# Optimization experiments

Hardware: AMD Instinct MI355X
Metric: run time of the kernel (lower is better)

The kernel has to match this reference:

```python
import jax, jax.numpy as jnp
import numpy as np
import math

NUM_HEADS = 8
DIM = 512
DH = DIM // NUM_HEADS  # 64


def _rotary(x):
    # x: (b, l, h, s, d) ; interleaved-pair rotary (lucidrains RotaryEmbedding default)
    d = x.shape[-1]
    s = x.shape[-2]
    inv_freq = 1.0 / (10000.0 ** (jnp.arange(0, d, 2, dtype=jnp.float32) / d))  # (d/2,)
    t = jnp.arange(s, dtype=jnp.float32)
    freqs = t[:, None] * inv_freq[None, :]                # (s, d/2)
    freqs = jnp.repeat(freqs, 2, axis=-1)                 # (s, d) interleaved duplication
    cos = jnp.cos(freqs).astype(x.dtype)
    sin = jnp.sin(freqs).astype(x.dtype)
    x1 = x[..., 0::2]
    x2 = x[..., 1::2]
    rot = jnp.stack([-x2, x1], axis=-1).reshape(x.shape)  # rotate_half on interleaved pairs
    return x * cos + rot * sin


def setup_inputs() -> dict:
    key = jax.random.key(0)
    ks = jax.random.split(key, 9)
    b, l, s = 2, 2, 2048
    std = 1.0 / math.sqrt(DIM)
    inp = {
        "x": jax.random.normal(ks[0], (b, l, s, DIM), dtype=jnp.float32),
        "Wq": jax.random.normal(ks[1], (DIM, DIM), dtype=jnp.float32) * std,
        "bq": jnp.zeros((DIM,), dtype=jnp.float32),
        "Wk": jax.random.normal(ks[2], (DIM, DIM), dtype=jnp.float32) * std,
        "bk": jnp.zeros((DIM,), dtype=jnp.float32),
        "Wv": jax.random.normal(ks[3], (DIM, DIM), dtype=jnp.float32) * std,
        "bv": jnp.zeros((DIM,), dtype=jnp.float32),
        "Wo": jax.random.normal(ks[4], (DIM, DIM), dtype=jnp.float32) * std,
        "bo": jnp.zeros((DIM,), dtype=jnp.float32),
    }
    return inp


def reference(x, Wq, bq, Wk, bk, Wv, bv, Wo, bo):
    b, l, s, _ = x.shape
    h, dh = NUM_HEADS, DH

    def proj(W, bias):
        y = jnp.einsum('blsd,ed->blse', x, W) + bias      # nn.Linear: x @ W.T + b
        return y.reshape(b, l, s, h, dh).transpose(0, 1, 3, 2, 4)  # b l h s d

    q_proj = proj(Wq, bq)
    k_proj = proj(Wk, bk)
    v_proj = proj(Wv, bv)

    # Faithful to the source's swapped tuple unpack: k_mat <- V projection, v_mat <- K projection
    q_mat = _rotary(q_proj)
    k_mat = _rotary(v_proj)
    v_mat = k_proj

    scale = 1.0 / math.sqrt(dh * h)  # sqrt(dim), as in source
    scores = jnp.einsum('blhqd,blhkd->blhqk', q_mat, k_mat) * scale

    causal = jnp.tril(jnp.ones((s, s), dtype=bool))
    scores = jnp.where(causal[None, None, None], scores, -jnp.inf)

    weights = jax.nn.softmax(scores, axis=-1)
    inter = jnp.einsum('blhqk,blhkd->blhqd', weights, v_mat)
    inter = inter.transpose(0, 1, 3, 2, 4).reshape(b, l, s, h * dh)  # b l s (h d)
    out = jnp.einsum('blse,de->blsd', inter, Wo) + bo
    return out
```

## Files before the change

kernel.cpp:

```cpp
#include <hip/hip_runtime.h>
#include <math.h>

#define BB 2
#define LL 2
#define SS 2048
#define DD 512
#define HH 8
#define DHH 64

typedef __attribute__((ext_vector_type(8))) short bf16x8;
typedef __attribute__((ext_vector_type(4))) float f32x4;

#define MFMA16(a, b, c) __builtin_amdgcn_mfma_f32_16x16x32_bf16((a), (b), (c), 0, 0, 0)

__device__ __forceinline__ unsigned short f2bf(float f) {
    union { float f; unsigned u; } x; x.f = f;
    unsigned u = x.u;
    return (unsigned short)((u + 0x7fffu + ((u >> 16) & 1u)) >> 16);
}

__device__ __forceinline__ void gload16(const unsigned short* g, unsigned short* l) {
    __builtin_amdgcn_global_load_lds(
        (const __attribute__((address_space(1))) unsigned int*)g,
        (__attribute__((address_space(3))) unsigned int*)l, 16, 0, 0);
}

__global__ void rope_table_kernel(float* __restrict__ cos_t, float* __restrict__ sin_t) {
    int idx = blockIdx.x * 256 + threadIdx.x;
    if (idx >= SS * 32) return;
    int s = idx >> 5;
    int f = idx & 31;
    double inv = pow(10000.0, -(double)(2 * f) / (double)DHH);
    double ang = (double)s * inv;
    cos_t[idx] = (float)cos(ang);
    sin_t[idx] = (float)sin(ang);
}

__global__ __launch_bounds__(256) void convert_kernel(
    const float* __restrict__ x,  const float* __restrict__ wq,
    const float* __restrict__ wk, const float* __restrict__ wv,
    const float* __restrict__ wo, unsigned short* __restrict__ dst)
{
    int i = blockIdx.x * 256 + threadIdx.x;
    const float* src;
    int local;
    if (i < 1048576)      { src = x;  local = i; }
    else if (i < 1114112) { src = wq; local = i - 1048576; }
    else if (i < 1179648) { src = wk; local = i - 1114112; }
    else if (i < 1245184) { src = wv; local = i - 1179648; }
    else                  { src = wo; local = i - 1245184; }
    float4 v = ((const float4*)src)[local];
    ushort4 o;
    o.x = f2bf(v.x); o.y = f2bf(v.y); o.z = f2bf(v.z); o.w = f2bf(v.w);
    *(ushort4*)&dst[(size_t)i * 4] = o;
}

__global__ __launch_bounds__(256) void qkv_mfma_kernel(
    const unsigned short* __restrict__ xb,
    const unsigned short* __restrict__ wqb,
    const unsigned short* __restrict__ wkb,
    const unsigned short* __restrict__ wvb,
    const float* __restrict__ bq, const float* __restrict__ bk,
    const float* __restrict__ bv,
    const float* __restrict__ cos_t, const float* __restrict__ sin_t,
    unsigned short* __restrict__ qm, unsigned short* __restrict__ km,
    unsigned short* __restrict__ vt)
{
    __shared__ __align__(16) unsigned short As[4096];
    __shared__ __align__(16) unsigned short Bs[4096];

    const int tid  = threadIdx.x;
    const int w    = tid >> 6;
    const int lane = tid & 63;
    const int c    = lane & 15;
    const int quad = lane >> 4;
    const int mw   = (w & 1) * 64;
    const int nw   = (w >> 1) * 64;

    const int bx    = blockIdx.x;
    const int mat   = bx >> 2;
    const int nloc0 = (bx & 3) * 128;
    const int row0  = blockIdx.y * 128;

    const unsigned short* wsel = (mat == 0) ? wqb : (mat == 1) ? wkb : wvb;
    const float* bsel          = (mat == 0) ? bq  : (mat == 1) ? bk  : bv;

    const unsigned short* aSrc = (mat == 1) ? (wsel + (size_t)nloc0 * DD)
                                            : (xb   + (size_t)row0  * DD);
    const unsigned short* bSrc = (mat == 1) ? (xb   + (size_t)row0  * DD)
                                            : (wsel + (size_t)nloc0 * DD);

    f32x4 acc[4][4];
    #pragma unroll
    for (int i = 0; i < 4; ++i)
        #pragma unroll
        for (int j = 0; j < 4; ++j)
            #pragma unroll
            for (int r = 0; r < 4; ++r) acc[i][j][r] = 0.f;

    for (int k0 = 0; k0 < DD; k0 += 32) {
        __syncthreads();
        #pragma unroll
        for (int it = 0; it < 2; ++it) {
            int L   = it * 2048 + w * 512 + lane * 8;
            int row = L >> 5;
            int k   = L & 31;
            gload16(aSrc + (size_t)row * DD + k0 + k, &As[L]);
            gload16(bSrc + (size_t)row * DD + k0 + k, &Bs[L]);
        }
        __syncthreads();
        bf16x8 af[4], bfr[4];
        #pragma unroll
        for (int mt = 0; mt < 4; ++mt)
            af[mt] = *(const bf16x8*)&As[(mw + mt * 16 + c) * 32 + quad * 8];
        #pragma unroll
        for (int nt = 0; nt < 4; ++nt)
            bfr[nt] = *(const bf16x8*)&Bs[(nw + nt * 16 + c) * 32 + quad * 8];
        #pragma unroll
        for (int mt = 0; mt < 4; ++mt)
            #pragma unroll
            for (int nt = 0; nt < 4; ++nt)
                acc[mt][nt] = MFMA16(af[mt], bfr[nt], acc[mt][nt]);
    }

    if (mat == 1) {
        #pragma unroll
        for (int mt = 0; mt < 4; ++mt) {
            #pragma unroll
            for (int nt = 0; nt < 4; ++nt) {
                int xr = row0 + nw + nt * 16 + c;
                int bl = xr >> 11, s = xr & 2047;
                #pragma unroll
                for (int r = 0; r < 4; ++r) {
                    int col = nloc0 + mw + mt * 16 + quad * 4 + r;
                    int h = col >> 6, dh = col & 63;
                    float v = acc[mt][nt][r] + bsel[col];
                    vt[((size_t)(bl * HH + h) * DHH + dh) * SS + s] = f2bf(v);
                }
            }
        }
    } else {
        unsigned short* dst = (mat == 0) ? qm : km;
        const float qscale = (mat == 0) ? 0.04419417382415922f : 1.0f;
        #pragma unroll
        for (int mt = 0; mt < 4; ++mt) {
            #pragma unroll
            for (int r = 0; r < 4; ++r) {
                int xr = row0 + mw + mt * 16 + quad * 4 + r;
                int bl = xr >> 11, s = xr & 2047;
                #pragma unroll
                for (int nt = 0; nt < 4; ++nt) {
                    int col = nloc0 + nw + nt * 16 + c;
                    int h = col >> 6, dh = col & 63;
                    float v = acc[mt][nt][r] + bsel[col];
                    float pv = __shfl_xor(v, 1);
                    int f = dh >> 1;
                    float cs = cos_t[s * 32 + f], sn = sin_t[s * 32 + f];
                    float o = (dh & 1) ? fmaf(v, cs, pv * sn)
                                       : fmaf(v, cs, -(pv * sn));
                    dst[((size_t)(bl * HH + h) * SS + s) * DHH + dh] = f2bf(o * qscale);
                }
            }
        }
    }
}

#define S_KV 72
#define S_P  72

__global__ __launch_bounds__(256) void attn_mfma_kernel(
    const unsigned short* __restrict__ qm,
    const unsigned short* __restrict__ km,
    const unsigned short* __restrict__ vt,
    unsigned short* __restrict__ inter)
{
    __shared__ unsigned short Ks[64 * S_KV];
    __shared__ unsigned short Vt[64 * S_KV];
    __shared__ unsigned short Ps[128 * S_P];

    const int tid  = threadIdx.x;
    const int w    = tid >> 6;
    const int lane = tid & 63;
    const int c    = lane & 15;
    const int quad = lane >> 4;

    const int qt = (gridDim.x - 1) - blockIdx.x;
    const int h  = blockIdx.y;
    const int bl = blockIdx.z;
    const int q0 = qt * 128;
    const int qw = q0 + w * 32;

    const size_t seq_base = (size_t)(bl * HH + h) * SS * DHH;
    const size_t vt_base  = (size_t)(bl * HH + h) * DHH * SS;

    bf16x8 qf[2][2];
    #pragma unroll
    for (int mt = 0; mt < 2; ++mt)
        #pragma unroll
        for (int kk = 0; kk < 2; ++kk)
            qf[mt][kk] = *(const bf16x8*)(qm + seq_base +
                (size_t)(qw + mt * 16 + c) * DHH + kk * 32 + quad * 8);

    f32x4 oacc[4][2];
    f32x4 lacc[2];
    #pragma unroll
    for (int i = 0; i < 4; ++i)
        #pragma unroll
        for (int j = 0; j < 2; ++j)
            #pragma unroll
            for (int r = 0; r < 4; ++r) oacc[i][j][r] = 0.f;
    #pragma unroll
    for (int j = 0; j < 2; ++j)
        #pragma unroll
        for (int r = 0; r < 4; ++r) lacc[j][r] = 0.f;

    bf16x8 ones;
    #pragma unroll
    for (int i = 0; i < 8; ++i) ones[i] = (short)0x3F80;

    const int ntiles = 2 * qt + 2;
    for (int kt = 0; kt < ntiles; ++kt) {
        __syncthreads();
        {
            const unsigned short* kg = km + seq_base + (size_t)(kt * 64) * DHH;
            const unsigned short* vg = vt + vt_base + kt * 64;
            #pragma unroll
            for (int it = 0; it < 2; ++it) {
                int idx = tid + it * 256;
                int row = idx >> 3, ch = idx & 7;
                *(bf16x8*)&Ks[row * S_KV + ch * 8] = *(const bf16x8*)(kg + idx * 8);
                *(bf16x8*)&Vt[row * S_KV + ch * 8] =
                    *(const bf16x8*)(vg + (size_t)row * SS + ch * 8);
            }
        }
        __syncthreads();

        if (64 * kt <= qw + 31) {
            f32x4 sacc[2][4];
            #pragma unroll
            for (int mt = 0; mt < 2; ++mt)
                #pragma unroll
                for (int nt = 0; nt < 4; ++nt)
                    #pragma unroll
                    for (int r = 0; r < 4; ++r) sacc[mt][nt][r] = 0.f;
            #pragma unroll
            for (int kk = 0; kk < 2; ++kk) {
                bf16x8 bk_[4];
                #pragma unroll
                for (int nt = 0; nt < 4; ++nt)
                    bk_[nt] = *(const bf16x8*)&Ks[(nt * 16 + c) * S_KV + kk * 32 + quad * 8];
                #pragma unroll
                for (int mt = 0; mt < 2; ++mt)
                    #pragma unroll
                    for (int nt = 0; nt < 4; ++nt)
                        sacc[mt][nt] = MFMA16(qf[mt][kk], bk_[nt], sacc[mt][nt]);
            }

            const bool need_mask = (64 * kt + 63 > qw);
            #pragma unroll
            for (int mt = 0; mt < 2; ++mt) {
                #pragma unroll
                for (int r = 0; r < 4; ++r) {
                    int prow = w * 32 + mt * 16 + quad * 4 + r;
                    int qrow = qw + mt * 16 + quad * 4 + r;
                    unsigned short* pp = &Ps[prow * S_P + c];
                    #pragma unroll
                    for (int nt = 0; nt < 4; ++nt) {
                        float p = __expf(sacc[mt][nt][r]);
                        if (need_mask && (64 * kt + nt * 16 + c > qrow)) p = 0.f;
                        pp[nt * 16] = f2bf(p);
                    }
                }
            }

            #pragma unroll
            for (int kk = 0; kk < 2; ++kk) {
                bf16x8 bp0 = *(const bf16x8*)&Ps[(w * 32 + c) * S_P + kk * 32 + quad * 8];
                bf16x8 bp1 = *(const bf16x8*)&Ps[(w * 32 + 16 + c) * S_P + kk * 32 + quad * 8];
                lacc[0] = MFMA16(ones, bp0, lacc[0]);
                lacc[1] = MFMA16(ones, bp1, lacc[1]);
                #pragma unroll
                for (int mt4 = 0; mt4 < 4; ++mt4) {
                    bf16x8 av = *(const bf16x8*)&Vt[(mt4 * 16 + c) * S_KV + kk * 32 + quad * 8];
                    oacc[mt4][0] = MFMA16(av, bp0, oacc[mt4][0]);
                    oacc[mt4][1] = MFMA16(av, bp1, oacc[mt4][1]);
                }
            }
        }
    }

    float invl0 = 1.f / lacc[0][0];
    float invl1 = 1.f / lacc[1][0];
    #pragma unroll
    for (int mt4 = 0; mt4 < 4; ++mt4) {
        int dh0 = mt4 * 16 + quad * 4;
        #pragma unroll
        for (int nt2 = 0; nt2 < 2; ++nt2) {
            int query = qw + nt2 * 16 + c;
            float il = nt2 ? invl1 : invl0;
            ushort4 o;
            o.x = f2bf(oacc[mt4][nt2][0] * il);
            o.y = f2bf(oacc[mt4][nt2][1] * il);
            o.z = f2bf(oacc[mt4][nt2][2] * il);
            o.w = f2bf(oacc[mt4][nt2][3] * il);
            *(ushort4*)&inter[((size_t)bl * SS + query) * DD + h * DHH + dh0] = o;
        }
    }
}

__global__ __launch_bounds__(256) void outproj_mfma_kernel(
    const unsigned short* __restrict__ ib,
    const unsigned short* __restrict__ wob,
    const float* __restrict__ bo, float* __restrict__ out)
{
    __shared__ __align__(16) unsigned short As[4096];
    __shared__ __align__(16) unsigned short Bs[4096];

    const int tid  = threadIdx.x;
    const int w    = tid >> 6;
    const int lane = tid & 63;
    const int c    = lane & 15;
    const int quad = lane >> 4;
    const int mw   = (w & 1) * 64;
    const int nw   = (w >> 1) * 64;

    const int n0   = blockIdx.x * 128;
    const int row0 = blockIdx.y * 128;

    const unsigned short* aSrc = ib  + (size_t)row0 * DD;
    const unsigned short* bSrc = wob + (size_t)n0   * DD;

    f32x4 acc[4][4];
    #pragma unroll
    for (int i = 0; i < 4; ++i)
        #pragma unroll
        for (int j = 0; j < 4; ++j)
            #pragma unroll
            for (int r = 0; r < 4; ++r) acc[i][j][r] = 0.f;

    for (int k0 = 0; k0 < DD; k0 += 32) {
        __syncthreads();
        #pragma unroll
        for (int it = 0; it < 2; ++it) {
            int L   = it * 2048 + w * 512 + lane * 8;
            int row = L >> 5;
            int k   = L & 31;
            gload16(aSrc + (size_t)row * DD + k0 + k, &As[L]);
            gload16(bSrc + (size_t)row * DD + k0 + k, &Bs[L]);
        }
        __syncthreads();
        bf16x8 af[4], bfr[4];
        #pragma unroll
        for (int mt = 0; mt < 4; ++mt)
            af[mt] = *(const bf16x8*)&As[(mw + mt * 16 + c) * 32 + quad * 8];
        #pragma unroll
        for (int nt = 0; nt < 4; ++nt)
            bfr[nt] = *(const bf16x8*)&Bs[(nw + nt * 16 + c) * 32 + quad * 8];
        #pragma unroll
        for (int mt = 0; mt < 4; ++mt)
            #pragma unroll
            for (int nt = 0; nt < 4; ++nt)
                acc[mt][nt] = MFMA16(af[mt], bfr[nt], acc[mt][nt]);
    }

    #pragma unroll
    for (int mt = 0; mt < 4; ++mt) {
        #pragma unroll
        for (int r = 0; r < 4; ++r) {
            int xr = row0 + mw + mt * 16 + quad * 4 + r;
            #pragma unroll
            for (int nt = 0; nt < 4; ++nt) {
                int col = n0 + nw + nt * 16 + c;
                out[(size_t)xr * DD + col] = acc[mt][nt][r] + bo[col];
            }
        }
    }
}

extern "C" void kernel_launch(void* const* d_in, const int* in_sizes, int n_in,
                              void* d_out, int out_size, void* d_ws, size_t ws_size,
                              hipStream_t stream)
{
    const float* x  = (const float*)d_in[0];
    const float* Wq = (const float*)d_in[1];
    const float* bq = (const float*)d_in[2];
    const float* Wk = (const float*)d_in[3];
    const float* bk = (const float*)d_in[4];
    const float* Wv = (const float*)d_in[5];
    const float* bv = (const float*)d_in[6];
    const float* Wo = (const float*)d_in[7];
    const float* bo = (const float*)d_in[8];
    float* out = (float*)d_out;
    char* ws = (char*)d_ws;

    unsigned short* inter = (unsigned short*)(ws);
    float* cos_t = (float*)(ws + 8388608);
    float* sin_t = (float*)(ws + 8650752);
    unsigned short* xb  = (unsigned short*)(ws + 8912896);
    unsigned short* wqb = (unsigned short*)(ws + 17301504);
    unsigned short* wkb = (unsigned short*)(ws + 17825792);
    unsigned short* wvb = (unsigned short*)(ws + 18350080);
    unsigned short* wob = (unsigned short*)(ws + 18874368);
    unsigned short* qm  = (unsigned short*)(ws + 19398656);
    unsigned short* km  = (unsigned short*)(ws + 27787264);
    unsigned short* vt  = (unsigned short*)(ws + 36175872);

    rope_table_kernel<<<dim3(256), dim3(256), 0, stream>>>(cos_t, sin_t);
    convert_kernel<<<dim3(5120), dim3(256), 0, stream>>>(x, Wq, Wk, Wv, Wo, xb);
    qkv_mfma_kernel<<<dim3(12, 64), dim3(256), 0, stream>>>(
        xb, wqb, wkb, wvb, bq, bk, bv, cos_t, sin_t, qm, km, vt);
    attn_mfma_kernel<<<dim3(16, HH, BB * LL), dim3(256), 0, stream>>>(qm, km, vt, inter);
    outproj_mfma_kernel<<<dim3(4, 64), dim3(256), 0, stream>>>(inter, wob, bo, out);
}
```

Baseline: 210.2 us.

## Restructure attention into single-wave blocks reading K/V directly from global

Rewrites the attention kernel so each 64-thread block handles 32 queries, loading K and V fragments straight from global memory instead of staging them in shared memory with block barriers. The grid grows to 2048 single-wave blocks ordered longest-first, which is meant to remove sync overhead and improve load balance on the causal triangle. It also folds log2(e) into the Q scale so exp2 can be used, computes S transposed (K as the A operand), and packs P to bf16 with a cheaper rounding and byte-permute store. The cost is that K/V tiles are no longer shared across waves, so global and L2 traffic rises, and the P conversion rounding changes slightly.

```diff
diff --git a/kernel.cpp b/kernel.cpp
--- a/kernel.cpp
+++ b/kernel.cpp
@@ -12,6 +12,12 @@
 typedef __attribute__((ext_vector_type(4))) float f32x4;
 
 #define MFMA16(a, b, c) __builtin_amdgcn_mfma_f32_16x16x32_bf16((a), (b), (c), 0, 0, 0)
+
+#if __has_builtin(__builtin_amdgcn_exp2f)
+#define EXP2F(x) __builtin_amdgcn_exp2f(x)
+#else
+#define EXP2F(x) __expf((x) * 0.6931471805599453f)
+#endif
 
 __device__ __forceinline__ unsigned short f2bf(float f) {
     union { float f; unsigned u; } x; x.f = f;
@@ -141,7 +147,7 @@
         }
     } else {
         unsigned short* dst = (mat == 0) ? qm : km;
-        const float qscale = (mat == 0) ? 0.04419417382415922f : 1.0f;
+        const float qscale = (mat == 0) ? 0.06375871448932861f : 1.0f;
         #pragma unroll
         for (int mt = 0; mt < 4; ++mt) {
             #pragma unroll
@@ -165,41 +171,35 @@
     }
 }
 
-#define S_KV 72
-#define S_P  72
-
-__global__ __launch_bounds__(256) void attn_mfma_kernel(
+#define S_P 72
+
+__global__ __launch_bounds__(64, 3) void attn_mfma_kernel(
     const unsigned short* __restrict__ qm,
     const unsigned short* __restrict__ km,
     const unsigned short* __restrict__ vt,
     unsigned short* __restrict__ inter)
 {
-    __shared__ unsigned short Ks[64 * S_KV];
-    __shared__ unsigned short Vt[64 * S_KV];
-    __shared__ unsigned short Ps[128 * S_P];
-
-    const int tid  = threadIdx.x;
-    const int w    = tid >> 6;
-    const int lane = tid & 63;
+    __shared__ __align__(16) unsigned short Ps[32 * S_P];
+
+    const int lane = threadIdx.x;
     const int c    = lane & 15;
     const int quad = lane >> 4;
 
-    const int qt = (gridDim.x - 1) - blockIdx.x;
-    const int h  = blockIdx.y;
-    const int bl = blockIdx.z;
-    const int q0 = qt * 128;
-    const int qw = q0 + w * 32;
+    const int g  = blockIdx.x;
+    const int h  = g & 7;
+    const int bl = (g >> 3) & 3;
+    const int qw = 32 * (63 - (g >> 5));
 
     const size_t seq_base = (size_t)(bl * HH + h) * SS * DHH;
     const size_t vt_base  = (size_t)(bl * HH + h) * DHH * SS;
 
     bf16x8 qf[2][2];
     #pragma unroll
-    for (int mt = 0; mt < 2; ++mt)
+    for (int nt = 0; nt < 2; ++nt)
         #pragma unroll
         for (int kk = 0; kk < 2; ++kk)
-            qf[mt][kk] = *(const bf16x8*)(qm + seq_base +
-                (size_t)(qw + mt * 16 + c) * DHH + kk * 32 + quad * 8);
+            qf[nt][kk] = *(const bf16x8*)(qm + seq_base +
+                (size_t)(qw + nt * 16 + c) * DHH + kk * 32 + quad * 8);
 
     f32x4 oacc[4][2];
     f32x4 lacc[2];
@@ -218,73 +218,69 @@
     #pragma unroll
     for (int i = 0; i < 8; ++i) ones[i] = (short)0x3F80;
 
-    const int ntiles = 2 * qt + 2;
+    const int ntiles = (qw >> 6) + 1;
     for (int kt = 0; kt < ntiles; ++kt) {
-        __syncthreads();
-        {
-            const unsigned short* kg = km + seq_base + (size_t)(kt * 64) * DHH;
-            const unsigned short* vg = vt + vt_base + kt * 64;
-            #pragma unroll
-            for (int it = 0; it < 2; ++it) {
-                int idx = tid + it * 256;
-                int row = idx >> 3, ch = idx & 7;
-                *(bf16x8*)&Ks[row * S_KV + ch * 8] = *(const bf16x8*)(kg + idx * 8);
-                *(bf16x8*)&Vt[row * S_KV + ch * 8] =
-                    *(const bf16x8*)(vg + (size_t)row * SS + ch * 8);
-            }
-        }
-        __syncthreads();
-
-        if (64 * kt <= qw + 31) {
-            f32x4 sacc[2][4];
-            #pragma unroll
-            for (int mt = 0; mt < 2; ++mt)
+        const unsigned short* kg = km + seq_base + (size_t)(kt * 64) * DHH;
+
+        f32x4 sacc[4][2];
+        #pragma unroll
+        for (int mt = 0; mt < 4; ++mt)
+            #pragma unroll
+            for (int nt = 0; nt < 2; ++nt)
                 #pragma unroll
-                for (int nt = 0; nt < 4; ++nt)
-                    #pragma unroll
-                    for (int r = 0; r < 4; ++r) sacc[mt][nt][r] = 0.f;
-            #pragma unroll
-            for (int kk = 0; kk < 2; ++kk) {
-                bf16x8 bk_[4];
+                for (int r = 0; r < 4; ++r) sacc[mt][nt][r] = 0.f;
+        #pragma unroll
+        for (int kk = 0; kk < 2; ++kk) {
+            bf16x8 kf[4];
+            #pragma unroll
+            for (int mt = 0; mt < 4; ++mt)
+                kf[mt] = *(const bf16x8*)(kg + (size_t)(mt * 16 + c) * DHH +
+                                          kk * 32 + quad * 8);
+            #pragma unroll
+            for (int mt = 0; mt < 4; ++mt)
                 #pragma unroll
-                for (int nt = 0; nt < 4; ++nt)
-                    bk_[nt] = *(const bf16x8*)&Ks[(nt * 16 + c) * S_KV + kk * 32 + quad * 8];
-                #pragma unroll
-                for (int mt = 0; mt < 2; ++mt)
-                    #pragma unroll
-                    for (int nt = 0; nt < 4; ++nt)
-                        sacc[mt][nt] = MFMA16(qf[mt][kk], bk_[nt], sacc[mt][nt]);
-            }
-
-            const bool need_mask = (64 * kt + 63 > qw);
-            #pragma unroll
-            for (int mt = 0; mt < 2; ++mt) {
+                for (int nt = 0; nt < 2; ++nt)
+                    sacc[mt][nt] = MFMA16(kf[mt], qf[nt][kk], sacc[mt][nt]);
+        }
+
+        const bool need_mask = (kt == ntiles - 1);
+        #pragma unroll
+        for (int mt = 0; mt < 4; ++mt) {
+            #pragma unroll
+            for (int nt = 0; nt < 2; ++nt) {
+                int q = qw + nt * 16 + c;
+                unsigned u[4];
                 #pragma unroll
                 for (int r = 0; r < 4; ++r) {
-                    int prow = w * 32 + mt * 16 + quad * 4 + r;
-                    int qrow = qw + mt * 16 + quad * 4 + r;
-                    unsigned short* pp = &Ps[prow * S_P + c];
-                    #pragma unroll
-                    for (int nt = 0; nt < 4; ++nt) {
-                        float p = __expf(sacc[mt][nt][r]);
-                        if (need_mask && (64 * kt + nt * 16 + c > qrow)) p = 0.f;
-                        pp[nt * 16] = f2bf(p);
+                    float p = EXP2F(sacc[mt][nt][r]);
+                    if (need_mask) {
+                        int key = kt * 64 + mt * 16 + quad * 4 + r;
+                        if (key > q) p = 0.f;
                     }
+                    union { float f; unsigned u; } cv; cv.f = p;
+                    u[r] = cv.u + 0x8000u;
                 }
-            }
-
-            #pragma unroll
-            for (int kk = 0; kk < 2; ++kk) {
-                bf16x8 bp0 = *(const bf16x8*)&Ps[(w * 32 + c) * S_P + kk * 32 + quad * 8];
-                bf16x8 bp1 = *(const bf16x8*)&Ps[(w * 32 + 16 + c) * S_P + kk * 32 + quad * 8];
-                lacc[0] = MFMA16(ones, bp0, lacc[0]);
-                lacc[1] = MFMA16(ones, bp1, lacc[1]);
-                #pragma unroll
-                for (int mt4 = 0; mt4 < 4; ++mt4) {
-                    bf16x8 av = *(const bf16x8*)&Vt[(mt4 * 16 + c) * S_KV + kk * 32 + quad * 8];
-                    oacc[mt4][0] = MFMA16(av, bp0, oacc[mt4][0]);
-                    oacc[mt4][1] = MFMA16(av, bp1, oacc[mt4][1]);
-                }
+                uint2 d;
+                d.x = __builtin_amdgcn_perm(u[1], u[0], 0x07060302u);
+                d.y = __builtin_amdgcn_perm(u[3], u[2], 0x07060302u);
+                *(uint2*)&Ps[(nt * 16 + c) * S_P + mt * 16 + quad * 4] = d;
+            }
+        }
+
+        #pragma unroll
+        for (int kk = 0; kk < 2; ++kk) {
+            bf16x8 bp[2];
+            #pragma unroll
+            for (int nt = 0; nt < 2; ++nt) {
+                bp[nt] = *(const bf16x8*)&Ps[(nt * 16 + c) * S_P + kk * 32 + quad * 8];
+                lacc[nt] = MFMA16(ones, bp[nt], lacc[nt]);
+            }
+            #pragma unroll
+            for (int mt4 = 0; mt4 < 4; ++mt4) {
+                bf16x8 av = *(const bf16x8*)(vt + vt_base +
+                    (size_t)(mt4 * 16 + c) * SS + kt * 64 + kk * 32 + quad * 8);
+                oacc[mt4][0] = MFMA16(av, bp[0], oacc[mt4][0]);
+                oacc[mt4][1] = MFMA16(av, bp[1], oacc[mt4][1]);
             }
         }
     }
@@ -295,14 +291,14 @@
     for (int mt4 = 0; mt4 < 4; ++mt4) {
         int dh0 = mt4 * 16 + quad * 4;
         #pragma unroll
-        for (int nt2 = 0; nt2 < 2; ++nt2) {
-            int query = qw + nt2 * 16 + c;
-            float il = nt2 ? invl1 : invl0;
+        for (int nt = 0; nt < 2; ++nt) {
+            int query = qw + nt * 16 + c;
+            float il = nt ? invl1 : invl0;
             ushort4 o;
-            o.x = f2bf(oacc[mt4][nt2][0] * il);
-            o.y = f2bf(oacc[mt4][nt2][1] * il);
-            o.z = f2bf(oacc[mt4][nt2][2] * il);
-            o.w = f2bf(oacc[mt4][nt2][3] * il);
+            o.x = f2bf(oacc[mt4][nt][0] * il);
+            o.y = f2bf(oacc[mt4][nt][1] * il);
+            o.z = f2bf(oacc[mt4][nt][2] * il);
+            o.w = f2bf(oacc[mt4][nt][3] * il);
             *(ushort4*)&inter[((size_t)bl * SS + query) * DD + h * DHH + dh0] = o;
         }
     }
@@ -409,6 +405,6 @@
     convert_kernel<<<dim3(5120), dim3(256), 0, stream>>>(x, Wq, Wk, Wv, Wo, xb);
     qkv_mfma_kernel<<<dim3(12, 64), dim3(256), 0, stream>>>(
         xb, wqb, wkb, wvb, bq, bk, bv, cos_t, sin_t, qm, km, vt);
-    attn_mfma_kernel<<<dim3(16, HH, BB * LL), dim3(256), 0, stream>>>(qm, km, vt, inter);
+    attn_mfma_kernel<<<dim3(2048), dim3(64), 0, stream>>>(qm, km, vt, inter);
     outproj_mfma_kernel<<<dim3(4, 64), dim3(256), 0, stream>>>(inter, wob, bo, out);
 }
```

New measurement: 228.6 us. +8.8%, slower.
